# Performance work log

Measured on AMD Instinct MI355X. Metric: run time of the kernel, lower is better.

## Reference

```python
import jax, jax.numpy as jnp
import numpy as np

EMBED = 1024
HEADS = 16
HEAD_DIM = EMBED // HEADS


def setup_inputs() -> dict:
    key = jax.random.key(0)
    ks = jax.random.split(key, 9)
    B, S = 1, 4096
    scale = 1.0 / np.sqrt(EMBED)
    x = jax.random.normal(ks[0], (B, S, EMBED), dtype=jnp.float32)
    # nn.Linear weights stored as [out, in]; we store transposed [in, out] for x @ W
    Wq = jax.random.uniform(ks[1], (EMBED, EMBED), jnp.float32, -scale, scale)
    bq = jax.random.uniform(ks[2], (EMBED,), jnp.float32, -scale, scale)
    Wk = jax.random.uniform(ks[3], (EMBED, EMBED), jnp.float32, -scale, scale)
    bk = jax.random.uniform(ks[4], (EMBED,), jnp.float32, -scale, scale)
    Wv = jax.random.uniform(ks[5], (EMBED, EMBED), jnp.float32, -scale, scale)
    bv = jax.random.uniform(ks[6], (EMBED,), jnp.float32, -scale, scale)
    Wo = jax.random.uniform(ks[7], (EMBED, EMBED), jnp.float32, -scale, scale)
    bo = jax.random.uniform(ks[8], (EMBED,), jnp.float32, -scale, scale)
    return {"x": x, "Wq": Wq, "bq": bq, "Wk": Wk, "bk": bk,
            "Wv": Wv, "bv": bv, "Wo": Wo, "bo": bo}


def reference(x, Wq, bq, Wk, bk, Wv, bv, Wo, bo):
    B, S, E = x.shape
    H, D = HEADS, HEAD_DIM
    # projections
    Q = (x @ Wq + bq).reshape(B, S, H, D).transpose(0, 2, 1, 3)  # [B,H,S,D]
    K = (x @ Wk + bk).reshape(B, S, H, D).transpose(0, 2, 1, 3)
    V = (x @ Wv + bv).reshape(B, S, H, D).transpose(0, 2, 1, 3)
    # unfused attention: full [B,H,S,S] score matrix, matching the torch module
    scores = jnp.einsum('bhqd,bhkd->bhqk', Q, K) / jnp.sqrt(jnp.float32(D)).astype(x.dtype)
    probs = jax.nn.softmax(scores, axis=-1)
    out = jnp.einsum('bhqk,bhkd->bhqd', probs, V)  # [B,H,S,D]
    out = out.transpose(0, 2, 1, 3).reshape(B, S, E)
    return out @ Wo + bo
```

## Files before the change

kernel.cpp:

```cpp
#include <hip/hip_runtime.h>


constexpr int Sq = 4096;
constexpr int Ee = 1024;
constexpr int Hh = 16;
constexpr int Dh = 64;

typedef _Float16 half8 __attribute__((ext_vector_type(8)));
typedef _Float16 half4 __attribute__((ext_vector_type(4)));
typedef _Float16 half2t __attribute__((ext_vector_type(2)));
typedef float f32x4 __attribute__((ext_vector_type(4)));

union U8 { half8 v8; half2t h2[4]; };

__device__ __forceinline__ unsigned short f2h(float f) {
  _Float16 h = (_Float16)f;
  return *reinterpret_cast<unsigned short*>(&h);
}

__device__ __forceinline__ half2t pk(float a, float b) {
  return __builtin_bit_cast(half2t, __builtin_amdgcn_cvt_pkrtz(a, b));
}

__device__ __forceinline__ void gload16(const void* g, void* l) {
  __builtin_amdgcn_global_load_lds(
      (const __attribute__((address_space(1))) void*)g,
      (__attribute__((address_space(3))) void*)l, 16, 0, 0);
}

__global__ void k_prep(const float* __restrict__ x,
                       const float* __restrict__ Wq, const float* __restrict__ Wk,
                       const float* __restrict__ Wv, const float* __restrict__ Wo,
                       unsigned short* __restrict__ xb,
                       unsigned short* __restrict__ Wqt, unsigned short* __restrict__ Wkt,
                       unsigned short* __restrict__ Wvt, unsigned short* __restrict__ Wot) {
  int b = blockIdx.x, t = threadIdx.x;
  if (b < 4096) {
    int i = b * 256 + t;
    float4 v = reinterpret_cast<const float4*>(x)[i];
    ushort4 o;
    o.x = f2h(v.x); o.y = f2h(v.y); o.z = f2h(v.z); o.w = f2h(v.w);
    reinterpret_cast<ushort4*>(xb)[i] = o;
    return;
  }
  __shared__ unsigned short tile[64][65];
  int r = b - 4096;
  int wi = r >> 8, ti = r & 255;
  const float* W = (wi == 0) ? Wq : (wi == 1) ? Wk : (wi == 2) ? Wv : Wo;
  unsigned short* Wt = (wi == 0) ? Wqt : (wi == 1) ? Wkt : (wi == 2) ? Wvt : Wot;
  int kb = (ti & 15) * 64, nb = (ti >> 4) * 64;
  int r0 = t >> 4, c4 = (t & 15) * 4;
  for (int i = 0; i < 4; i++) {
    int row = r0 + i * 16;
    float4 v = *reinterpret_cast<const float4*>(W + (size_t)(kb + row) * Ee + nb + c4);
    tile[row][c4 + 0] = f2h(v.x); tile[row][c4 + 1] = f2h(v.y);
    tile[row][c4 + 2] = f2h(v.z); tile[row][c4 + 3] = f2h(v.w);
  }
  __syncthreads();
  for (int i = 0; i < 4; i++) {
    int nrow = r0 + i * 16;
    ushort4 o;
    o.x = tile[c4 + 0][nrow]; o.y = tile[c4 + 1][nrow];
    o.z = tile[c4 + 2][nrow]; o.w = tile[c4 + 3][nrow];
    *reinterpret_cast<ushort4*>(Wt + (size_t)(nb + nrow) * Ee + kb + c4) = o;
  }
}

template <bool TR>
__device__ __forceinline__ void gemm_kloop(
    const unsigned short* __restrict__ A, const unsigned short* __restrict__ Wt,
    unsigned short* Al, unsigned short* Bl,
    int m0, int n0, int t, int wm, int wn, int quad, int c, f32x4 (&acc)[4][4]) {
  for (int k0 = 0; k0 < 1024; k0 += 64) {
    __syncthreads();
#pragma unroll
    for (int i = 0; i < 4; i++) {
      int ch = i * 256 + t;
      int row = ch >> 3, kg = (ch & 7) ^ (row & 7);
      gload16(A + (size_t)(m0 + row) * 1024 + k0 + kg * 8, &Al[ch * 8]);
    }
#pragma unroll
    for (int i = 0; i < 4; i++) {
      int ch = i * 256 + t;
      int row = ch >> 3, kg = (ch & 7) ^ (row & 7);
      gload16(Wt + (size_t)(n0 + row) * 1024 + k0 + kg * 8, &Bl[ch * 8]);
    }
    __syncthreads();
#pragma unroll
    for (int ks = 0; ks < 2; ks++) {
      half8 af[4], bfr[4];
#pragma unroll
      for (int i = 0; i < 4; i++) {
        int row = wm * 64 + i * 16 + c;
        int kg = (quad + 4 * ks) ^ (row & 7);
        af[i] = *reinterpret_cast<const half8*>(&Al[row * 64 + kg * 8]);
      }
#pragma unroll
      for (int j = 0; j < 4; j++) {
        int row = wn * 64 + j * 16 + c;
        int kg = (quad + 4 * ks) ^ (row & 7);
        bfr[j] = *reinterpret_cast<const half8*>(&Bl[row * 64 + kg * 8]);
      }
#pragma unroll
      for (int i = 0; i < 4; i++)
#pragma unroll
        for (int j = 0; j < 4; j++) {
          if (TR)
            acc[j][i] = __builtin_amdgcn_mfma_f32_16x16x32_f16(bfr[j], af[i], acc[j][i], 0, 0, 0);
          else
            acc[i][j] = __builtin_amdgcn_mfma_f32_16x16x32_f16(af[i], bfr[j], acc[i][j], 0, 0, 0);
        }
    }
  }
}

__global__ __launch_bounds__(256) void k_gemm(
    const unsigned short* __restrict__ A,
    const unsigned short* __restrict__ W0, const unsigned short* __restrict__ W1,
    const unsigned short* __restrict__ W2,
    const float* __restrict__ b0, const float* __restrict__ b1, const float* __restrict__ b2,
    void* d0, void* d1, void* d2) {
  __shared__ __align__(16) unsigned short Al[128 * 64];
  __shared__ __align__(16) unsigned short Bl[128 * 64];
  const unsigned short* Wt; const float* bias; void* dst;
  if (blockIdx.z == 0)      { Wt = W0; bias = b0; dst = d0; }
  else if (blockIdx.z == 1) { Wt = W1; bias = b1; dst = d1; }
  else                      { Wt = W2; bias = b2; dst = d2; }

  int t = threadIdx.x;
  int w = t >> 6, L = t & 63, quad = L >> 4, c = L & 15;
  int m0 = blockIdx.x * 128, n0 = blockIdx.y * 128;
  int wm = w >> 1, wn = w & 1;

  f32x4 zero = {0.f, 0.f, 0.f, 0.f};
  f32x4 acc[4][4];
#pragma unroll
  for (int i = 0; i < 4; i++)
#pragma unroll
    for (int j = 0; j < 4; j++) acc[i][j] = zero;

  if (blockIdx.z < 2) gemm_kloop<true>(A, Wt, Al, Bl, m0, n0, t, wm, wn, quad, c, acc);
  else                gemm_kloop<false>(A, Wt, Al, Bl, m0, n0, t, wm, wn, quad, c, acc);

  if (blockIdx.z < 2) {
    float sc = (blockIdx.z == 0) ? 0.18033688011112042f : 1.0f;
    unsigned short* qk = (unsigned short*)dst;
#pragma unroll
    for (int j = 0; j < 4; j++) {
      int nb4 = n0 + wn * 64 + j * 16 + quad * 4;
      int hh = nb4 >> 6, d = nb4 & 63;
      f32x4 b4 = *reinterpret_cast<const f32x4*>(bias + nb4);
#pragma unroll
      for (int i = 0; i < 4; i++) {
        int s = m0 + wm * 64 + i * 16 + c;
        half4 hv;
#pragma unroll
        for (int r = 0; r < 4; r++) hv[r] = (_Float16)((acc[j][i][r] + b4[r]) * sc);
        *reinterpret_cast<half4*>(&qk[(size_t)hh * Sq * Dh + (size_t)s * Dh + d]) = hv;
      }
    }
    return;
  }
  unsigned short* Vt = (unsigned short*)dst;
#pragma unroll
  for (int j = 0; j < 4; j++) {
    int n = n0 + wn * 64 + j * 16 + c;
    int hh = n >> 6, d = n & 63;
    float bv = bias[n];
#pragma unroll
    for (int i = 0; i < 4; i++) {
      int pos = m0 + wm * 64 + (i >> 1) * 32 + quad * 8 + (i & 1) * 4;
      half4 hv;
#pragma unroll
      for (int r = 0; r < 4; r++) hv[r] = (_Float16)(acc[i][j][r] + bv);
      *reinterpret_cast<half4*>(&Vt[(size_t)hh * Dh * Sq + (size_t)d * Sq + pos]) = hv;
    }
  }
}

__global__ __launch_bounds__(256) void k_gemmO(
    const unsigned short* __restrict__ A, const unsigned short* __restrict__ Wt,
    const float* __restrict__ bias, float* __restrict__ out) {
  __shared__ __align__(16) unsigned short Al[64 * 64];
  __shared__ __align__(16) unsigned short Bl[128 * 64];
  int t = threadIdx.x;
  int w = t >> 6, L = t & 63, quad = L >> 4, c = L & 15;
  int m0 = blockIdx.x * 64, n0 = blockIdx.y * 128;
  int wm = w & 1, wn = w >> 1;

  f32x4 zero = {0.f, 0.f, 0.f, 0.f};
  f32x4 acc[4][2];
#pragma unroll
  for (int j = 0; j < 4; j++)
#pragma unroll
    for (int i = 0; i < 2; i++) acc[j][i] = zero;

  for (int k0 = 0; k0 < 1024; k0 += 64) {
    __syncthreads();
#pragma unroll
    for (int i = 0; i < 2; i++) {
      int ch = i * 256 + t;
      int row = ch >> 3, kg = (ch & 7) ^ (row & 7);
      gload16(A + (size_t)(m0 + row) * 1024 + k0 + kg * 8, &Al[ch * 8]);
    }
#pragma unroll
    for (int i = 0; i < 4; i++) {
      int ch = i * 256 + t;
      int row = ch >> 3, kg = (ch & 7) ^ (row & 7);
      gload16(Wt + (size_t)(n0 + row) * 1024 + k0 + kg * 8, &Bl[ch * 8]);
    }
    __syncthreads();
#pragma unroll
    for (int ks = 0; ks < 2; ks++) {
      half8 af[2], bfr[4];
#pragma unroll
      for (int i = 0; i < 2; i++) {
        int row = wm * 32 + i * 16 + c;
        int kg = (quad + 4 * ks) ^ (row & 7);
        af[i] = *reinterpret_cast<const half8*>(&Al[row * 64 + kg * 8]);
      }
#pragma unroll
      for (int j = 0; j < 4; j++) {
        int row = wn * 64 + j * 16 + c;
        int kg = (quad + 4 * ks) ^ (row & 7);
        bfr[j] = *reinterpret_cast<const half8*>(&Bl[row * 64 + kg * 8]);
      }
#pragma unroll
      for (int j = 0; j < 4; j++)
#pragma unroll
        for (int i = 0; i < 2; i++)
          acc[j][i] = __builtin_amdgcn_mfma_f32_16x16x32_f16(bfr[j], af[i], acc[j][i], 0, 0, 0);
    }
  }

#pragma unroll
  for (int j = 0; j < 4; j++) {
    int nb4 = n0 + wn * 64 + j * 16 + quad * 4;
    f32x4 b4 = *reinterpret_cast<const f32x4*>(bias + nb4);
#pragma unroll
    for (int i = 0; i < 2; i++) {
      int s = m0 + wm * 32 + i * 16 + c;
      f32x4 v = acc[j][i] + b4;
      *reinterpret_cast<f32x4*>(out + (size_t)s * 1024 + nb4) = v;
    }
  }
}

__global__ __launch_bounds__(256, 2) void k_attn(
    const unsigned short* __restrict__ Q, const unsigned short* __restrict__ K,
    const unsigned short* __restrict__ Vt, unsigned short* __restrict__ O) {
  __shared__ __align__(16) unsigned short SM[32768];
  int t = threadIdx.x;
  int w = t >> 6, L = t & 63, quad = L >> 4, c = L & 15;
  int wl = w & 1, par = w >> 1;
  int h = blockIdx.y, qb = blockIdx.x;
  const unsigned short* Qh = Q + (size_t)h * Sq * Dh;
  const unsigned short* Kh = K + (size_t)h * Sq * Dh;
  const unsigned short* Vth = Vt + (size_t)h * Dh * Sq;

  half8 qf[4][2];
#pragma unroll
  for (int qg = 0; qg < 4; qg++) {
    int qrow = qb * 128 + wl * 64 + qg * 16 + c;
#pragma unroll
    for (int ks = 0; ks < 2; ks++)
      qf[qg][ks] = *reinterpret_cast<const half8*>(Qh + (size_t)qrow * Dh + ks * 32 + quad * 8);
  }

  f32x4 zero = {0.f, 0.f, 0.f, 0.f};
  f32x4 o[4][4];
  f32x4 l[4];
#pragma unroll
  for (int qg = 0; qg < 4; qg++) {
    l[qg] = zero;
#pragma unroll
    for (int dt = 0; dt < 4; dt++) o[qg][dt] = zero;
  }
  half8 ones8;
#pragma unroll
  for (int j = 0; j < 8; j++) ones8[j] = (_Float16)1.0f;

  int koff[2][4], voff[4][2];
#pragma unroll
  for (int ks = 0; ks < 2; ks++)
#pragma unroll
    for (int nt = 0; nt < 4; nt++) {
      int row = nt * 16 + c;
      koff[ks][nt] = par * 4096 + row * 64 + (((ks * 4 + quad) ^ (row & 7)) * 8);
    }
#pragma unroll
  for (int dt = 0; dt < 4; dt++)
#pragma unroll
    for (int n2 = 0; n2 < 2; n2++) {
      int row = dt * 16 + c;
      voff[dt][n2] = (2 + par) * 4096 + row * 64 + (((n2 * 4 + quad) ^ (row & 7)) * 8);
    }

  const unsigned short* KgB[2];
  const unsigned short* VgB[2];
#pragma unroll
  for (int i = 0; i < 2; i++) {
    int ch = i * 256 + t;
    int row = ch >> 3, kg = (ch & 7) ^ (row & 7);
    KgB[i] = Kh + row * Dh + kg * 8;
    VgB[i] = Vth + (size_t)row * Sq + kg * 8;
  }

  auto stage = [&](int bufo, int tb) {
#pragma unroll
    for (int p2 = 0; p2 < 2; p2++) {
#pragma unroll
      for (int i = 0; i < 2; i++)
        gload16(KgB[i] + (size_t)(tb + p2) * 4096, &SM[bufo + p2 * 4096 + (i * 256 + t) * 8]);
#pragma unroll
      for (int i = 0; i < 2; i++)
        gload16(VgB[i] + (size_t)(tb + p2) * 64, &SM[bufo + (2 + p2) * 4096 + (i * 256 + t) * 8]);
    }
  };

  stage(0, 0);

  auto body = [&](int BUFOFF) {
    half8 pB[4][2];
#pragma unroll
    for (int h2 = 0; h2 < 2; h2++) {
      f32x4 st[2][4];
#pragma unroll
      for (int q2 = 0; q2 < 2; q2++)
#pragma unroll
        for (int nt = 0; nt < 4; nt++) st[q2][nt] = zero;
      __builtin_amdgcn_s_setprio(1);
#pragma unroll
      for (int ks = 0; ks < 2; ks++)
#pragma unroll
        for (int nt = 0; nt < 4; nt++) {
          half8 kfv = *reinterpret_cast<const half8*>(&SM[koff[ks][nt] + BUFOFF]);
          st[0][nt] = __builtin_amdgcn_mfma_f32_16x16x32_f16(kfv, qf[2 * h2 + 0][ks], st[0][nt], 0, 0, 0);
          st[1][nt] = __builtin_amdgcn_mfma_f32_16x16x32_f16(kfv, qf[2 * h2 + 1][ks], st[1][nt], 0, 0, 0);
        }
      __builtin_amdgcn_s_setprio(0);
#pragma unroll
      for (int q2 = 0; q2 < 2; q2++)
#pragma unroll
        for (int n2 = 0; n2 < 2; n2++) {
          U8 u;
          u.h2[0] = pk(__builtin_amdgcn_exp2f(st[q2][2 * n2][0]), __builtin_amdgcn_exp2f(st[q2][2 * n2][1]));
          u.h2[1] = pk(__builtin_amdgcn_exp2f(st[q2][2 * n2][2]), __builtin_amdgcn_exp2f(st[q2][2 * n2][3]));
          u.h2[2] = pk(__builtin_amdgcn_exp2f(st[q2][2 * n2 + 1][0]), __builtin_amdgcn_exp2f(st[q2][2 * n2 + 1][1]));
          u.h2[3] = pk(__builtin_amdgcn_exp2f(st[q2][2 * n2 + 1][2]), __builtin_amdgcn_exp2f(st[q2][2 * n2 + 1][3]));
          pB[2 * h2 + q2][n2] = u.v8;
          l[2 * h2 + q2] = __builtin_amdgcn_mfma_f32_16x16x32_f16(ones8, u.v8, l[2 * h2 + q2], 0, 0, 0);
        }
    }
    __builtin_amdgcn_s_setprio(1);
#pragma unroll
    for (int dt = 0; dt < 4; dt++)
#pragma unroll
      for (int n2 = 0; n2 < 2; n2++) {
        half8 vv = *reinterpret_cast<const half8*>(&SM[voff[dt][n2] + BUFOFF]);
        o[0][dt] = __builtin_amdgcn_mfma_f32_16x16x32_f16(vv, pB[0][n2], o[0][dt], 0, 0, 0);
        o[1][dt] = __builtin_amdgcn_mfma_f32_16x16x32_f16(vv, pB[1][n2], o[1][dt], 0, 0, 0);
        o[2][dt] = __builtin_amdgcn_mfma_f32_16x16x32_f16(vv, pB[2][n2], o[2][dt], 0, 0, 0);
        o[3][dt] = __builtin_amdgcn_mfma_f32_16x16x32_f16(vv, pB[3][n2], o[3][dt], 0, 0, 0);
      }
    __builtin_amdgcn_s_setprio(0);
  };

  for (int ob2 = 0; ob2 < 16; ob2++) {
    __syncthreads();
    stage(16384, 4 * ob2 + 2);
    body(0);
    __syncthreads();
    if (ob2 < 15) stage(0, 4 * ob2 + 4);
    body(16384);
  }

  __syncthreads();
  float* cb = (float*)SM;
  if (par == 1) {
#pragma unroll
    for (int qg = 0; qg < 4; qg++)
#pragma unroll
      for (int dt = 0; dt < 4; dt++)
        *reinterpret_cast<f32x4*>(cb + ((wl * 17 + qg * 4 + dt) * 64 + L) * 4) = o[qg][dt];
    f32x4 lv = {l[0][0], l[1][0], l[2][0], l[3][0]};
    *reinterpret_cast<f32x4*>(cb + ((wl * 17 + 16) * 64 + L) * 4) = lv;
  }
  __syncthreads();
  if (par == 0) {
#pragma unroll
    for (int qg = 0; qg < 4; qg++)
#pragma unroll
      for (int dt = 0; dt < 4; dt++)
        o[qg][dt] += *reinterpret_cast<const f32x4*>(cb + ((wl * 17 + qg * 4 + dt) * 64 + L) * 4);
    f32x4 lv = *reinterpret_cast<const f32x4*>(cb + ((wl * 17 + 16) * 64 + L) * 4);
#pragma unroll
    for (int qg = 0; qg < 4; qg++) {
      float inv = 1.f / (l[qg][0] + lv[qg]);
      int q = qb * 128 + wl * 64 + qg * 16 + c;
#pragma unroll
      for (int dt = 0; dt < 4; dt++) {
        half4 hv;
#pragma unroll
        for (int r = 0; r < 4; r++) hv[r] = (_Float16)(o[qg][dt][r] * inv);
        *reinterpret_cast<half4*>(&O[(size_t)q * 1024 + h * 64 + dt * 16 + quad * 4]) = hv;
      }
    }
  }
}

extern "C" void kernel_launch(void* const* d_in, const int* in_sizes, int n_in,
                              void* d_out, int out_size, void* d_ws, size_t ws_size,
                              hipStream_t stream) {
  const float* x  = (const float*)d_in[0];
  const float* Wq = (const float*)d_in[1];
  const float* bq = (const float*)d_in[2];
  const float* Wk = (const float*)d_in[3];
  const float* bk = (const float*)d_in[4];
  const float* Wv = (const float*)d_in[5];
  const float* bv = (const float*)d_in[6];
  const float* Wo = (const float*)d_in[7];
  const float* bo = (const float*)d_in[8];

  char* ws = (char*)d_ws;
  const size_t MB = 1u << 20;
  unsigned short* xb  = (unsigned short*)(ws);
  unsigned short* Wqt = (unsigned short*)(ws + 8 * MB);
  unsigned short* Wkt = (unsigned short*)(ws + 10 * MB);
  unsigned short* Wvt = (unsigned short*)(ws + 12 * MB);
  unsigned short* Wot = (unsigned short*)(ws + 14 * MB);
  unsigned short* Qb  = (unsigned short*)(ws + 16 * MB);
  unsigned short* Kb  = (unsigned short*)(ws + 24 * MB);
  unsigned short* Vtg = (unsigned short*)(ws + 32 * MB);
  unsigned short* Ob  = (unsigned short*)(ws + 40 * MB);

  k_prep<<<5120, 256, 0, stream>>>(x, Wq, Wk, Wv, Wo, xb, Wqt, Wkt, Wvt, Wot);
  k_gemm<<<dim3(32, 8, 3), 256, 0, stream>>>(xb, Wqt, Wkt, Wvt, bq, bk, bv,
                                             (void*)Qb, (void*)Kb, (void*)Vtg);
  k_attn<<<dim3(32, 16), 256, 0, stream>>>(Qb, Kb, Vtg, Ob);
  k_gemmO<<<dim3(64, 8), 256, 0, stream>>>(Ob, Wot, bo, (float*)d_out);
}
```

Baseline: 219.9 us.

## Interleave exp/pack of one query half with MFMAs of the other half

```diff
diff --git a/kernel.cpp b/kernel.cpp
--- a/kernel.cpp
+++ b/kernel.cpp
@@ -320,49 +320,69 @@
 
   stage(0, 0);
 
+  auto packu = [&](f32x4 (&stq)[4], int n2, half8 (&pBq)[2], f32x4& lq) {
+    U8 u;
+    u.h2[0] = pk(__builtin_amdgcn_exp2f(stq[2 * n2][0]), __builtin_amdgcn_exp2f(stq[2 * n2][1]));
+    u.h2[1] = pk(__builtin_amdgcn_exp2f(stq[2 * n2][2]), __builtin_amdgcn_exp2f(stq[2 * n2][3]));
+    u.h2[2] = pk(__builtin_amdgcn_exp2f(stq[2 * n2 + 1][0]), __builtin_amdgcn_exp2f(stq[2 * n2 + 1][1]));
+    u.h2[3] = pk(__builtin_amdgcn_exp2f(stq[2 * n2 + 1][2]), __builtin_amdgcn_exp2f(stq[2 * n2 + 1][3]));
+    pBq[n2] = u.v8;
+    lq = __builtin_amdgcn_mfma_f32_16x16x32_f16(ones8, u.v8, lq, 0, 0, 0);
+  };
+
   auto body = [&](int BUFOFF) {
-    half8 pB[4][2];
-#pragma unroll
-    for (int h2 = 0; h2 < 2; h2++) {
-      f32x4 st[2][4];
-#pragma unroll
-      for (int q2 = 0; q2 < 2; q2++)
-#pragma unroll
-        for (int nt = 0; nt < 4; nt++) st[q2][nt] = zero;
-      __builtin_amdgcn_s_setprio(1);
-#pragma unroll
-      for (int ks = 0; ks < 2; ks++)
-#pragma unroll
-        for (int nt = 0; nt < 4; nt++) {
-          half8 kfv = *reinterpret_cast<const half8*>(&SM[koff[ks][nt] + BUFOFF]);
-          st[0][nt] = __builtin_amdgcn_mfma_f32_16x16x32_f16(kfv, qf[2 * h2 + 0][ks], st[0][nt], 0, 0, 0);
-          st[1][nt] = __builtin_amdgcn_mfma_f32_16x16x32_f16(kfv, qf[2 * h2 + 1][ks], st[1][nt], 0, 0, 0);
-        }
-      __builtin_amdgcn_s_setprio(0);
-#pragma unroll
-      for (int q2 = 0; q2 < 2; q2++)
-#pragma unroll
-        for (int n2 = 0; n2 < 2; n2++) {
-          U8 u;
-          u.h2[0] = pk(__builtin_amdgcn_exp2f(st[q2][2 * n2][0]), __builtin_amdgcn_exp2f(st[q2][2 * n2][1]));
-          u.h2[1] = pk(__builtin_amdgcn_exp2f(st[q2][2 * n2][2]), __builtin_amdgcn_exp2f(st[q2][2 * n2][3]));
-          u.h2[2] = pk(__builtin_amdgcn_exp2f(st[q2][2 * n2 + 1][0]), __builtin_amdgcn_exp2f(st[q2][2 * n2 + 1][1]));
-          u.h2[3] = pk(__builtin_amdgcn_exp2f(st[q2][2 * n2 + 1][2]), __builtin_amdgcn_exp2f(st[q2][2 * n2 + 1][3]));
-          pB[2 * h2 + q2][n2] = u.v8;
-          l[2 * h2 + q2] = __builtin_amdgcn_mfma_f32_16x16x32_f16(ones8, u.v8, l[2 * h2 + q2], 0, 0, 0);
-        }
-    }
+    half8 pB0[2][2], pB1[2][2];
+    f32x4 stA[2][4], stB[2][4];
+#pragma unroll
+    for (int q2 = 0; q2 < 2; q2++)
+#pragma unroll
+      for (int nt = 0; nt < 4; nt++) stA[q2][nt] = zero;
     __builtin_amdgcn_s_setprio(1);
 #pragma unroll
-    for (int dt = 0; dt < 4; dt++)
-#pragma unroll
-      for (int n2 = 0; n2 < 2; n2++) {
-        half8 vv = *reinterpret_cast<const half8*>(&SM[voff[dt][n2] + BUFOFF]);
-        o[0][dt] = __builtin_amdgcn_mfma_f32_16x16x32_f16(vv, pB[0][n2], o[0][dt], 0, 0, 0);
-        o[1][dt] = __builtin_amdgcn_mfma_f32_16x16x32_f16(vv, pB[1][n2], o[1][dt], 0, 0, 0);
-        o[2][dt] = __builtin_amdgcn_mfma_f32_16x16x32_f16(vv, pB[2][n2], o[2][dt], 0, 0, 0);
-        o[3][dt] = __builtin_amdgcn_mfma_f32_16x16x32_f16(vv, pB[3][n2], o[3][dt], 0, 0, 0);
-      }
+    for (int ks = 0; ks < 2; ks++)
+#pragma unroll
+      for (int nt = 0; nt < 4; nt++) {
+        half8 kfv = *reinterpret_cast<const half8*>(&SM[koff[ks][nt] + BUFOFF]);
+        stA[0][nt] = __builtin_amdgcn_mfma_f32_16x16x32_f16(kfv, qf[0][ks], stA[0][nt], 0, 0, 0);
+        stA[1][nt] = __builtin_amdgcn_mfma_f32_16x16x32_f16(kfv, qf[1][ks], stA[1][nt], 0, 0, 0);
+      }
+    __builtin_amdgcn_s_setprio(0);
+#pragma unroll
+    for (int q2 = 0; q2 < 2; q2++)
+#pragma unroll
+      for (int nt = 0; nt < 4; nt++) stB[q2][nt] = zero;
+#pragma unroll
+    for (int s = 0; s < 8; s++) {
+      int ks = s >> 2, nt = s & 3;
+      half8 kfv = *reinterpret_cast<const half8*>(&SM[koff[ks][nt] + BUFOFF]);
+      stB[0][nt] = __builtin_amdgcn_mfma_f32_16x16x32_f16(kfv, qf[2][ks], stB[0][nt], 0, 0, 0);
+      stB[1][nt] = __builtin_amdgcn_mfma_f32_16x16x32_f16(kfv, qf[3][ks], stB[1][nt], 0, 0, 0);
+      if (s & 1) {
+        int u = s >> 1, q2 = u >> 1, n2 = u & 1;
+        packu(stA[q2], n2, pB0[q2], l[q2]);
+      }
+      __builtin_amdgcn_sched_barrier(0x3F4);
+    }
+#pragma unroll
+    for (int s = 0; s < 8; s++) {
+      int dt = s >> 1, n2 = s & 1;
+      half8 vv = *reinterpret_cast<const half8*>(&SM[voff[dt][n2] + BUFOFF]);
+      o[0][dt] = __builtin_amdgcn_mfma_f32_16x16x32_f16(vv, pB0[0][n2], o[0][dt], 0, 0, 0);
+      o[1][dt] = __builtin_amdgcn_mfma_f32_16x16x32_f16(vv, pB0[1][n2], o[1][dt], 0, 0, 0);
+      if (s & 1) {
+        int u = s >> 1, q2 = u >> 1, n2b = u & 1;
+        packu(stB[q2], n2b, pB1[q2], l[2 + q2]);
+      }
+      __builtin_amdgcn_sched_barrier(0x3F4);
+    }
+    __builtin_amdgcn_s_setprio(1);
+#pragma unroll
+    for (int s = 0; s < 8; s++) {
+      int dt = s >> 1, n2 = s & 1;
+      half8 vv = *reinterpret_cast<const half8*>(&SM[voff[dt][n2] + BUFOFF]);
+      o[2][dt] = __builtin_amdgcn_mfma_f32_16x16x32_f16(vv, pB1[0][n2], o[2][dt], 0, 0, 0);
+      o[3][dt] = __builtin_amdgcn_mfma_f32_16x16x32_f16(vv, pB1[1][n2], o[3][dt], 0, 0, 0);
+    }
     __builtin_amdgcn_s_setprio(0);
   };
 
```

After: 226.6 us. +3.1%, slower.
